# Performance work log

Measured on AMD Instinct MI355X. Metric: run time of the kernel, lower is better.

Reference implementation:

```python
import jax, jax.numpy as jnp
import numpy as np

DIM = 192; HEADS = 6; WS = 7; RES = 56; SHIFT = 3
HEAD_DIM = DIM // HEADS
SCALE = HEAD_DIM ** -0.5
N = WS * WS
EPS = 1e-5

def _rel_pos_index():
    coords = np.stack(np.meshgrid(np.arange(WS), np.arange(WS), indexing='ij')).reshape(2, -1)
    rel = coords[:, :, None] - coords[:, None, :]  # [2,N,N]
    rel = rel.transpose(1, 2, 0)
    rel[:, :, 0] += WS - 1
    rel[:, :, 1] += WS - 1
    rel[:, :, 0] *= 2 * WS - 1
    return rel.sum(-1)  # [N,N]

def _attn_mask():
    img = np.zeros((RES, RES), dtype=np.float32)
    slices = (slice(0, -WS), slice(-WS, -SHIFT), slice(-SHIFT, None))
    cnt = 0
    for h in slices:
        for w in slices:
            img[h, w] = cnt; cnt += 1
    mw = img.reshape(RES // WS, WS, RES // WS, WS).transpose(0, 2, 1, 3).reshape(-1, N)  # [nW,N]
    diff = mw[:, None, :] - mw[:, :, None]
    return np.where(diff != 0, -100.0, 0.0).astype(np.float32)  # [nW,N,N]

REL_IDX = jnp.asarray(_rel_pos_index())
ATTN_MASK = jnp.asarray(_attn_mask())

def _ln(x, g, b):
    mu = x.mean(-1, keepdims=True)
    var = ((x - mu) ** 2).mean(-1, keepdims=True)
    return (x - mu) * jax.lax.rsqrt(var + EPS) * g + b

def setup_inputs() -> dict:
    key = jax.random.key(0)
    ks = jax.random.split(key, 8)
    d = {
        'x': jax.random.normal(ks[0], (32, RES * RES, DIM), jnp.float32),
        'norm1_g': jnp.ones((DIM,), jnp.float32), 'norm1_b': jnp.zeros((DIM,), jnp.float32),
        'qkv_w': jax.random.normal(ks[1], (DIM, 3 * DIM), jnp.float32) * 0.02,
        'qkv_b': jnp.zeros((3 * DIM,), jnp.float32),
        'proj_w': jax.random.normal(ks[2], (DIM, DIM), jnp.float32) * 0.02,
        'proj_b': jnp.zeros((DIM,), jnp.float32),
        'bias_table': jax.random.normal(ks[3], ((2 * WS - 1) ** 2, HEADS), jnp.float32) * 0.02,
        'norm2_g': jnp.ones((DIM,), jnp.float32), 'norm2_b': jnp.zeros((DIM,), jnp.float32),
        'fc1_w': jax.random.normal(ks[4], (DIM, 4 * DIM), jnp.float32) * 0.02,
        'fc1_b': jnp.zeros((4 * DIM,), jnp.float32),
        'fc2_w': jax.random.normal(ks[5], (4 * DIM, DIM), jnp.float32) * 0.02,
        'fc2_b': jnp.zeros((DIM,), jnp.float32),
    }
    return d

def reference(x, norm1_g, norm1_b, qkv_w, qkv_b, proj_w, proj_b, bias_table,
              norm2_g, norm2_b, fc1_w, fc1_b, fc2_w, fc2_b):
    B, L, C = x.shape
    H = W = RES
    shortcut = x
    h = _ln(x, norm1_g, norm1_b).reshape(B, H, W, C)
    # cyclic shift
    h = jnp.roll(h, (-SHIFT, -SHIFT), axis=(1, 2))
    # window partition -> [B*nW, N, C]
    nH = H // WS
    h = h.reshape(B, nH, WS, nH, WS, C).transpose(0, 1, 3, 2, 4, 5).reshape(-1, N, C)
    BW = h.shape[0]
    # windowed MHSA
    qkv = (h @ qkv_w + qkv_b).reshape(BW, N, 3, HEADS, HEAD_DIM)
    q, k, v = qkv[:, :, 0], qkv[:, :, 1], qkv[:, :, 2]  # [BW,N,h,hd]
    attn = jnp.einsum('bnhd,bmhd->bhnm', q, k) * SCALE  # [BW,h,N,N]
    bias = bias_table[REL_IDX.reshape(-1)].reshape(N, N, HEADS).transpose(2, 0, 1)
    attn = attn + bias[None]
    nW = ATTN_MASK.shape[0]
    attn = attn.reshape(BW // nW, nW, HEADS, N, N) + ATTN_MASK[None, :, None]
    attn = jax.nn.softmax(attn.reshape(BW, HEADS, N, N), axis=-1)
    h = jnp.einsum('bhnm,bmhd->bnhd', attn, v).reshape(BW, N, C)
    h = h @ proj_w + proj_b
    # window reverse
    h = h.reshape(B, nH, nH, WS, WS, C).transpose(0, 1, 3, 2, 4, 5).reshape(B, H, W, C)
    h = jnp.roll(h, (SHIFT, SHIFT), axis=(1, 2)).reshape(B, L, C)
    x = shortcut + h
    # MLP
    m = _ln(x, norm2_g, norm2_b)
    m = jax.nn.gelu(m @ fc1_w + fc1_b, approximate=False) @ fc2_w + fc2_b
    return x + m
```

## Files before the change

### kernel.cpp

```cpp
#include <hip/hip_runtime.h>
#include <hip/hip_bf16.h>
#include <math.h>

typedef __attribute__((ext_vector_type(8))) short bh8;
typedef __attribute__((ext_vector_type(4))) float fx4;

__device__ __forceinline__ fx4 mfma_bf16(bh8 a, bh8 b, fx4 c) {
    return __builtin_amdgcn_mfma_f32_16x16x32_bf16(a, b, c, 0, 0, 0);
}

__device__ __forceinline__ void gload16(const __hip_bfloat16* g, __hip_bfloat16* l) {
    __builtin_amdgcn_global_load_lds(
        (const __attribute__((address_space(1))) void*)g,
        (__attribute__((address_space(3))) void*)l,
        16, 0, 0);
}

__device__ __forceinline__ float fast_erf(float u) {
    float au = fabsf(u);
    float t  = __builtin_amdgcn_rcpf(1.0f + 0.3275911f * au);
    float p  = ((((1.061405429f * t - 1.453152027f) * t + 1.421413741f) * t
                 - 0.284496736f) * t + 0.254829592f) * t;
    float e  = __expf(-u * u);
    return copysignf(1.0f - p * e, u);
}

#define WAITV8 do { asm volatile("s_waitcnt vmcnt(8)" ::: "memory"); \
                    __builtin_amdgcn_sched_barrier(0); } while (0)
#define WAITV0 do { asm volatile("s_waitcnt vmcnt(0)" ::: "memory"); \
                    __builtin_amdgcn_sched_barrier(0); } while (0)
#define LGKM0  do { asm volatile("s_waitcnt lgkmcnt(0)" ::: "memory"); \
                    __builtin_amdgcn_sched_barrier(0); } while (0)
#define BARR   do { __builtin_amdgcn_s_barrier(); \
                    __builtin_amdgcn_sched_barrier(0); } while (0)

__global__ __launch_bounds__(256)
void convw_k(const float* __restrict__ W, __hip_bfloat16* __restrict__ Wt, int K, int Nn)
{
    int idx = blockIdx.x * 256 + threadIdx.x;
    if (idx < K * Nn) {
        int k = idx / Nn, n = idx - k * Nn;
        Wt[(size_t)n * K + k] = __float2bfloat16(W[idx]);
    }
}

__global__ __launch_bounds__(256)
void ln1_gather_k(const float* __restrict__ x, const float* __restrict__ g,
                  const float* __restrict__ bia, __hip_bfloat16* __restrict__ xw)
{
    const int wave = threadIdx.x >> 6, lane = threadIdx.x & 63;
    const int t = blockIdx.x * 4 + wave;
    const int w = t / 49, n = t - w * 49;
    const int b = w >> 6, wrem = w & 63, wi = wrem >> 3, wj = wrem & 7;
    const int i = n / 7, j = n - i * 7;
    int sr = wi * 7 + i + 3; if (sr >= 56) sr -= 56;
    int sc = wj * 7 + j + 3; if (sc >= 56) sc -= 56;
    const float* xp = x + ((size_t)b * 3136 + sr * 56 + sc) * 192;
    float v0 = xp[lane], v1 = xp[lane + 64], v2 = xp[lane + 128];
    float s = v0 + v1 + v2;
    float q = v0 * v0 + v1 * v1 + v2 * v2;
    for (int off = 32; off > 0; off >>= 1) {
        s += __shfl_down(s, off, 64);
        q += __shfl_down(q, off, 64);
    }
    s = __shfl(s, 0, 64); q = __shfl(q, 0, 64);
    float mean = s * (1.0f / 192.0f);
    float var  = q * (1.0f / 192.0f) - mean * mean;
    float rstd = rsqrtf(var + 1e-5f);
    __hip_bfloat16* op = xw + (size_t)t * 192;
    op[lane]       = __float2bfloat16((v0 - mean) * rstd * g[lane]       + bia[lane]);
    op[lane + 64]  = __float2bfloat16((v1 - mean) * rstd * g[lane + 64]  + bia[lane + 64]);
    op[lane + 128] = __float2bfloat16((v2 - mean) * rstd * g[lane + 128] + bia[lane + 128]);
}

template<int MODE, int K, int NOUT>
__global__ __launch_bounds__(256)
void gemm2_k(const __hip_bfloat16* __restrict__ A,
             const __hip_bfloat16* __restrict__ Bt,
             const float* __restrict__ bias,
             const float* __restrict__ resid,
             void* __restrict__ outv)
{
    __shared__ __align__(16) __hip_bfloat16 As[128 * 32];
    __shared__ __align__(16) __hip_bfloat16 Bs[64 * 32];
    const int tid  = threadIdx.x;
    const int lane = tid & 63, wave = tid >> 6;
    const int quad = lane >> 4, l15 = lane & 15;
    const int m0 = blockIdx.x * 128, n0 = blockIdx.y * 64;

    const int arow = lane >> 2, acol = (lane & 3) * 8;
    const __hip_bfloat16* Ag0 = A  + (size_t)(m0 + wave * 32 + arow)      * K + acol;
    const __hip_bfloat16* Ag1 = A  + (size_t)(m0 + wave * 32 + 16 + arow) * K + acol;
    const __hip_bfloat16* Bg  = Bt + (size_t)(n0 + wave * 16 + arow)      * K + acol;
    __hip_bfloat16* Al0 = &As[(wave * 32)      * 32];
    __hip_bfloat16* Al1 = &As[(wave * 32 + 16) * 32];
    __hip_bfloat16* Bl  = &Bs[(wave * 16)      * 32];

    fx4 acc[2][4];
#pragma unroll
    for (int mi = 0; mi < 2; mi++)
#pragma unroll
        for (int ni = 0; ni < 4; ni++) acc[mi][ni] = {0.f, 0.f, 0.f, 0.f};

    for (int k0 = 0; k0 < K; k0 += 32) {
        gload16(Ag0 + k0, Al0);
        gload16(Ag1 + k0, Al1);
        gload16(Bg  + k0, Bl);
        __syncthreads();
        bh8 a0 = *(const bh8*)&As[(wave * 32 + l15)      * 32 + quad * 8];
        bh8 a1 = *(const bh8*)&As[(wave * 32 + 16 + l15) * 32 + quad * 8];
        bh8 b0 = *(const bh8*)&Bs[(0 * 16 + l15) * 32 + quad * 8];
        bh8 b1 = *(const bh8*)&Bs[(1 * 16 + l15) * 32 + quad * 8];
        bh8 b2 = *(const bh8*)&Bs[(2 * 16 + l15) * 32 + quad * 8];
        bh8 b3 = *(const bh8*)&Bs[(3 * 16 + l15) * 32 + quad * 8];
        acc[0][0] = mfma_bf16(a0, b0, acc[0][0]);
        acc[0][1] = mfma_bf16(a0, b1, acc[0][1]);
        acc[0][2] = mfma_bf16(a0, b2, acc[0][2]);
        acc[0][3] = mfma_bf16(a0, b3, acc[0][3]);
        acc[1][0] = mfma_bf16(a1, b0, acc[1][0]);
        acc[1][1] = mfma_bf16(a1, b1, acc[1][1]);
        acc[1][2] = mfma_bf16(a1, b2, acc[1][2]);
        acc[1][3] = mfma_bf16(a1, b3, acc[1][3]);
        __syncthreads();
    }

#pragma unroll
    for (int mi = 0; mi < 2; mi++)
#pragma unroll
    for (int ni = 0; ni < 4; ni++) {
        const int n = n0 + ni * 16 + l15;
        const float bn = bias[n];
#pragma unroll
        for (int r = 0; r < 4; r++) {
            const int m = m0 + wave * 32 + mi * 16 + quad * 4 + r;
            float v = acc[mi][ni][r] + bn;
            if (MODE == 0) {
                if (n < 192) v *= 0.17677669529663687f;
                ((__hip_bfloat16*)outv)[(size_t)m * NOUT + n] = __float2bfloat16(v);
            } else if (MODE == 2) {
                v = 0.5f * v * (1.0f + erff(v * 0.70710678118654752f));
                ((__hip_bfloat16*)outv)[(size_t)m * NOUT + n] = __float2bfloat16(v);
            } else {
                ((float*)outv)[(size_t)m * NOUT + n] = v + resid[(size_t)m * NOUT + n];
            }
        }
    }
}

__global__ __launch_bounds__(256)
void mlp_k(const __hip_bfloat16* __restrict__ A,
           const __hip_bfloat16* __restrict__ W1t,
           const __hip_bfloat16* __restrict__ W2t,
           const float* __restrict__ b1,
           const float* __restrict__ b2,
           float* __restrict__ out)
{
    __shared__ __align__(16) __hip_bfloat16 W1s[2][6][32][32];
    __shared__ __align__(16) __hip_bfloat16 W2s[2][192][32];
    __shared__ __align__(16) __hip_bfloat16 Hs[64][40];

    const int tid  = threadIdx.x;
    const int lane = tid & 63, wave = tid >> 6;
    const int quad = lane >> 4, l15 = lane & 15;
    const int m0 = blockIdx.x * 64;
    const int arow = lane >> 2, acol = (lane & 3) * 8;

    bh8 xr[6];
    const __hip_bfloat16* xg = A + (size_t)(m0 + wave * 16 + l15) * 192 + quad * 8;
#pragma unroll
    for (int kc = 0; kc < 6; kc++) xr[kc] = *(const bh8*)(xg + kc * 32);

    auto stage = [&](int bf, int c) {
#pragma unroll
        for (int i = 0; i < 3; i++) {
            const int g = wave * 3 + i;
            const int kc = g >> 1, half = g & 1;
            gload16(W1t + (size_t)(c * 32 + half * 16 + arow) * 192 + kc * 32 + acol,
                    &W1s[bf][kc][half * 16][0]);
            gload16(W2t + (size_t)(g * 16 + arow) * 768 + c * 32 + acol,
                    &W2s[bf][g * 16][0]);
        }
    };

    fx4 acc2[12];
#pragma unroll
    for (int nt = 0; nt < 12; nt++) acc2[nt] = {0.f, 0.f, 0.f, 0.f};

    stage(0, 0);
    float b1a0 = b1[l15],      b1a1 = b1[16 + l15];
    stage(1, 1);
    float b1b0 = b1[32 + l15], b1b1 = b1[48 + l15];
    float b1c0 = 0.f, b1c1 = 0.f;

    int cur = 0;
    for (int c = 0; c < 23; ++c) {
        WAITV8;
        BARR;

        fx4 acc1[2];
        acc1[0] = {0.f, 0.f, 0.f, 0.f};
        acc1[1] = {0.f, 0.f, 0.f, 0.f};
        __builtin_amdgcn_s_setprio(1);
#pragma unroll
        for (int kc = 0; kc < 6; kc++) {
#pragma unroll
            for (int ni = 0; ni < 2; ni++) {
                bh8 b = *(const bh8*)&W1s[cur][kc][ni * 16 + l15][quad * 8];
                acc1[ni] = mfma_bf16(xr[kc], b, acc1[ni]);
            }
        }
        __builtin_amdgcn_s_setprio(0);

#pragma unroll
        for (int ni = 0; ni < 2; ni++) {
            const float bb = ni ? b1a1 : b1a0;
#pragma unroll
            for (int r = 0; r < 4; r++) {
                float v = acc1[ni][r] + bb;
                float h = 0.5f * v * (1.0f + fast_erf(v * 0.70710678118654752f));
                Hs[wave * 16 + quad * 4 + r][ni * 16 + l15] = __float2bfloat16(h);
            }
        }
        LGKM0;

        bh8 ap = *(const bh8*)&Hs[wave * 16 + l15][quad * 8];
        __builtin_amdgcn_s_setprio(1);
#pragma unroll
        for (int nt = 0; nt < 12; nt++) {
            bh8 b = *(const bh8*)&W2s[cur][nt * 16 + l15][quad * 8];
            acc2[nt] = mfma_bf16(ap, b, acc2[nt]);
        }
        __builtin_amdgcn_s_setprio(0);

        BARR;
        if (c < 22) {
            stage(cur, c + 2);
            b1c0 = b1[(c + 2) * 32 + l15];
            b1c1 = b1[(c + 2) * 32 + 16 + l15];
        }
        b1a0 = b1b0; b1a1 = b1b1;
        b1b0 = b1c0; b1b1 = b1c1;
        cur ^= 1;
    }

    {
        WAITV0;
        BARR;
        fx4 acc1[2];
        acc1[0] = {0.f, 0.f, 0.f, 0.f};
        acc1[1] = {0.f, 0.f, 0.f, 0.f};
#pragma unroll
        for (int kc = 0; kc < 6; kc++) {
#pragma unroll
            for (int ni = 0; ni < 2; ni++) {
                bh8 b = *(const bh8*)&W1s[cur][kc][ni * 16 + l15][quad * 8];
                acc1[ni] = mfma_bf16(xr[kc], b, acc1[ni]);
            }
        }
#pragma unroll
        for (int ni = 0; ni < 2; ni++) {
            const float bb = ni ? b1a1 : b1a0;
#pragma unroll
            for (int r = 0; r < 4; r++) {
                float v = acc1[ni][r] + bb;
                float h = 0.5f * v * (1.0f + fast_erf(v * 0.70710678118654752f));
                Hs[wave * 16 + quad * 4 + r][ni * 16 + l15] = __float2bfloat16(h);
            }
        }
        LGKM0;
        bh8 ap = *(const bh8*)&Hs[wave * 16 + l15][quad * 8];
#pragma unroll
        for (int nt = 0; nt < 12; nt++) {
            bh8 b = *(const bh8*)&W2s[cur][nt * 16 + l15][quad * 8];
            acc2[nt] = mfma_bf16(ap, b, acc2[nt]);
        }
    }

#pragma unroll
    for (int nt = 0; nt < 12; nt++) {
        const int n = nt * 16 + l15;
        const float bn = b2[n];
#pragma unroll
        for (int r = 0; r < 4; r++) {
            const int m = m0 + wave * 16 + quad * 4 + r;
            out[(size_t)m * 192 + n] += acc2[nt][r] + bn;
        }
    }
}

__global__ __launch_bounds__(256)
void projln_k(const __hip_bfloat16* __restrict__ A,
              const __hip_bfloat16* __restrict__ Bt,
              const float* __restrict__ pb,
              const float* __restrict__ xresid,
              const float* __restrict__ g2,
              const float* __restrict__ b2,
              float* __restrict__ x1out,
              __hip_bfloat16* __restrict__ y2out)
{
    __shared__ __align__(16) __hip_bfloat16 As[64 * 32];
    __shared__ __align__(16) __hip_bfloat16 Bs[192 * 32];
    const int tid  = threadIdx.x;
    const int lane = tid & 63, wave = tid >> 6;
    const int quad = lane >> 4, l15 = lane & 15;
    const int m0 = blockIdx.x * 64;

    const int arow = lane >> 2, acol = (lane & 3) * 8;
    const __hip_bfloat16* Ag = A + (size_t)(m0 + wave * 16 + arow) * 192 + acol;
    __hip_bfloat16* Al = &As[(wave * 16) * 32];
    const __hip_bfloat16* Bg0 = Bt + (size_t)((wave + 0) * 16 + arow) * 192 + acol;
    const __hip_bfloat16* Bg1 = Bt + (size_t)((wave + 4) * 16 + arow) * 192 + acol;
    const __hip_bfloat16* Bg2 = Bt + (size_t)((wave + 8) * 16 + arow) * 192 + acol;
    __hip_bfloat16* Bl0 = &Bs[((wave + 0) * 16) * 32];
    __hip_bfloat16* Bl1 = &Bs[((wave + 4) * 16) * 32];
    __hip_bfloat16* Bl2 = &Bs[((wave + 8) * 16) * 32];

    fx4 acc[12];
#pragma unroll
    for (int ct = 0; ct < 12; ct++) acc[ct] = {0.f, 0.f, 0.f, 0.f};

    for (int k0 = 0; k0 < 192; k0 += 32) {
        gload16(Ag  + k0, Al);
        gload16(Bg0 + k0, Bl0);
        gload16(Bg1 + k0, Bl1);
        gload16(Bg2 + k0, Bl2);
        __syncthreads();
        bh8 a = *(const bh8*)&As[(wave * 16 + l15) * 32 + quad * 8];
#pragma unroll
        for (int ct = 0; ct < 12; ct++) {
            bh8 b = *(const bh8*)&Bs[(ct * 16 + l15) * 32 + quad * 8];
            acc[ct] = mfma_bf16(a, b, acc[ct]);
        }
        __syncthreads();
    }

#pragma unroll
    for (int r = 0; r < 4; r++) {
        const int row = m0 + wave * 16 + quad * 4 + r;
        float vv[12];
        float s = 0.f, q = 0.f;
#pragma unroll
        for (int ct = 0; ct < 12; ct++) {
            const int col = ct * 16 + l15;
            float v = acc[ct][r] + pb[col] + xresid[(size_t)row * 192 + col];
            vv[ct] = v;
            x1out[(size_t)row * 192 + col] = v;
            s += v;
            q += v * v;
        }
        s += __shfl_xor(s, 1, 64);  q += __shfl_xor(q, 1, 64);
        s += __shfl_xor(s, 2, 64);  q += __shfl_xor(q, 2, 64);
        s += __shfl_xor(s, 4, 64);  q += __shfl_xor(q, 4, 64);
        s += __shfl_xor(s, 8, 64);  q += __shfl_xor(q, 8, 64);
        float mean = s * (1.0f / 192.0f);
        float var  = q * (1.0f / 192.0f) - mean * mean;
        float rstd = rsqrtf(var + 1e-5f);
#pragma unroll
        for (int ct = 0; ct < 12; ct++) {
            const int col = ct * 16 + l15;
            float y = (vv[ct] - mean) * rstd * g2[col] + b2[col];
            y2out[(size_t)row * 192 + col] = __float2bfloat16(y);
        }
    }
}

__global__ __launch_bounds__(256)
void attn_k(const __hip_bfloat16* __restrict__ qkv,
            const float* __restrict__ bias_table,
            __hip_bfloat16* __restrict__ aout)
{
    __shared__ __align__(16) __hip_bfloat16 Qb[64 * 32];
    __shared__ __align__(16) __hip_bfloat16 Kb[64 * 32];
    __shared__ __align__(16) __hip_bfloat16 Vt[32 * 64];
    __shared__ __align__(16) __hip_bfloat16 Ps[64 * 72];
    __shared__ float bias_h[169];

    const int tid  = threadIdx.x;
    const int lane = tid & 63, wave = tid >> 6;
    const int quad = lane >> 4, l15 = lane & 15;
    const int w = blockIdx.x / 6, hd = blockIdx.x % 6;
    const int b = w >> 6, wrem = w & 63, wi = wrem >> 3, wj = wrem & 7;
    const size_t base = (size_t)w * 49 * 576 + hd * 32;

    if (tid < 169) bias_h[tid] = bias_table[tid * 6 + hd];

    bh8 z = {0, 0, 0, 0, 0, 0, 0, 0};
    {
        int row = tid >> 2, ch = (tid & 3) * 8;
        if (row < 49) {
            *(bh8*)&Qb[row * 32 + ch] = *(const bh8*)(qkv + base + (size_t)row * 576 + ch);
            *(bh8*)&Kb[row * 32 + ch] = *(const bh8*)(qkv + base + (size_t)row * 576 + 192 + ch);
        } else {
            *(bh8*)&Qb[row * 32 + ch] = z;
            *(bh8*)&Kb[row * 32 + ch] = z;
        }
        *(bh8*)&Vt[tid * 8] = z;
    }
    __syncthreads();
    for (int idx = tid; idx < 49 * 32; idx += 256) {
        int n = idx >> 5, d = idx & 31;
        Vt[d * 64 + n] = qkv[base + (size_t)n * 576 + 384 + d];
    }
    __syncthreads();

    fx4 zf = {0.f, 0.f, 0.f, 0.f};
    bh8 aq = *(const bh8*)&Qb[(wave * 16 + l15) * 32 + quad * 8];
    fx4 sarr[4];
#pragma unroll
    for (int ni = 0; ni < 4; ni++) {
        bh8 bk = *(const bh8*)&Kb[(ni * 16 + l15) * 32 + quad * 8];
        sarr[ni] = mfma_bf16(aq, bk, zf);
    }

    int iarr[4], ria[4], cia[4], mbi[4];
#pragma unroll
    for (int r = 0; r < 4; r++) {
        int i = wave * 16 + quad * 4 + r;
        int ri = i / 7, ci = i - ri * 7;
        iarr[r] = i; ria[r] = ri; cia[r] = ci;
        int ar = wi * 7 + ri, ac = wj * 7 + ci;
        int br = (ar < 49) ? 0 : ((ar < 53) ? 1 : 2);
        int bc = (ac < 49) ? 0 : ((ac < 53) ? 1 : 2);
        mbi[r] = br * 3 + bc;
    }
    float vals[4][4];
#pragma unroll
    for (int ni = 0; ni < 4; ni++) {
        int jcol = ni * 16 + l15;
        int rj = jcol / 7, cj = jcol - rj * 7;
        int ar = wi * 7 + rj, ac = wj * 7 + cj;
        int br = (ar < 49) ? 0 : ((ar < 53) ? 1 : 2);
        int bc = (ac < 49) ? 0 : ((ac < 53) ? 1 : 2);
        int mbj = br * 3 + bc;
#pragma unroll
        for (int r = 0; r < 4; r++) {
            float v;
            if (jcol >= 49)            v = -1e30f;
            else if (iarr[r] >= 49)    v = 0.0f;
            else {
                int bidx = (ria[r] - rj + 6) * 13 + (cia[r] - cj + 6);
                v = sarr[ni][r] + bias_h[bidx] + ((mbi[r] != mbj) ? -100.0f : 0.0f);
            }
            vals[ni][r] = v;
        }
    }
#pragma unroll
    for (int r = 0; r < 4; r++) {
        float mx = fmaxf(fmaxf(vals[0][r], vals[1][r]), fmaxf(vals[2][r], vals[3][r]));
        mx = fmaxf(mx, __shfl_xor(mx, 1, 64));
        mx = fmaxf(mx, __shfl_xor(mx, 2, 64));
        mx = fmaxf(mx, __shfl_xor(mx, 4, 64));
        mx = fmaxf(mx, __shfl_xor(mx, 8, 64));
        float e0 = __expf(vals[0][r] - mx);
        float e1 = __expf(vals[1][r] - mx);
        float e2 = __expf(vals[2][r] - mx);
        float e3 = __expf(vals[3][r] - mx);
        float sm = e0 + e1 + e2 + e3;
        sm += __shfl_xor(sm, 1, 64);
        sm += __shfl_xor(sm, 2, 64);
        sm += __shfl_xor(sm, 4, 64);
        sm += __shfl_xor(sm, 8, 64);
        float inv = 1.0f / sm;
        int prow = (wave * 16 + quad * 4 + r) * 72;
        Ps[prow + 0 * 16 + l15] = __float2bfloat16(e0 * inv);
        Ps[prow + 1 * 16 + l15] = __float2bfloat16(e1 * inv);
        Ps[prow + 2 * 16 + l15] = __float2bfloat16(e2 * inv);
        Ps[prow + 3 * 16 + l15] = __float2bfloat16(e3 * inv);
    }
    __syncthreads();

    fx4 o0 = zf, o1 = zf;
#pragma unroll
    for (int k0 = 0; k0 < 64; k0 += 32) {
        bh8 ap  = *(const bh8*)&Ps[(wave * 16 + l15) * 72 + k0 + quad * 8];
        bh8 bv0 = *(const bh8*)&Vt[(l15)      * 64 + k0 + quad * 8];
        bh8 bv1 = *(const bh8*)&Vt[(16 + l15) * 64 + k0 + quad * 8];
        o0 = mfma_bf16(ap, bv0, o0);
        o1 = mfma_bf16(ap, bv1, o1);
    }

#pragma unroll
    for (int r = 0; r < 4; r++) {
        int m = wave * 16 + quad * 4 + r;
        if (m < 49) {
            int i = m / 7, j2 = m - i * 7;
            int orow = wi * 7 + i + 3;  if (orow >= 56) orow -= 56;
            int ocol = wj * 7 + j2 + 3; if (ocol >= 56) ocol -= 56;
            size_t t = (size_t)b * 3136 + orow * 56 + ocol;
            aout[t * 192 + hd * 32 + l15]      = __float2bfloat16(o0[r]);
            aout[t * 192 + hd * 32 + 16 + l15] = __float2bfloat16(o1[r]);
        }
    }
}

extern "C" void kernel_launch(void* const* d_in, const int* in_sizes, int n_in,
                              void* d_out, int out_size, void* d_ws, size_t ws_size,
                              hipStream_t stream)
{
    const float* x      = (const float*)d_in[0];
    const float* n1g    = (const float*)d_in[1];
    const float* n1b    = (const float*)d_in[2];
    const float* qkv_w  = (const float*)d_in[3];
    const float* qkv_b  = (const float*)d_in[4];
    const float* proj_w = (const float*)d_in[5];
    const float* proj_b = (const float*)d_in[6];
    const float* btab   = (const float*)d_in[7];
    const float* n2g    = (const float*)d_in[8];
    const float* n2b    = (const float*)d_in[9];
    const float* fc1_w  = (const float*)d_in[10];
    const float* fc1_b  = (const float*)d_in[11];
    const float* fc2_w  = (const float*)d_in[12];
    const float* fc2_b  = (const float*)d_in[13];

    char* ws = (char*)d_ws;
    __hip_bfloat16* buf1    = (__hip_bfloat16*)(ws + 0);
    __hip_bfloat16* buf2    = (__hip_bfloat16*)(ws + 38535168);
    __hip_bfloat16* wt_qkv  = (__hip_bfloat16*)(ws + 192675840);
    __hip_bfloat16* wt_proj = (__hip_bfloat16*)(ws + 192897024);
    __hip_bfloat16* wt_fc1  = (__hip_bfloat16*)(ws + 192970752);
    __hip_bfloat16* wt_fc2  = (__hip_bfloat16*)(ws + 193265664);
    float*          x1      = (float*)d_out;

    convw_k<<<dim3(432), 256, 0, stream>>>(qkv_w, wt_qkv, 192, 576);
    convw_k<<<dim3(144), 256, 0, stream>>>(proj_w, wt_proj, 192, 192);
    convw_k<<<dim3(576), 256, 0, stream>>>(fc1_w, wt_fc1, 192, 768);
    convw_k<<<dim3(576), 256, 0, stream>>>(fc2_w, wt_fc2, 768, 192);

    ln1_gather_k<<<dim3(25088), 256, 0, stream>>>(x, n1g, n1b, buf1);

    gemm2_k<0, 192, 576><<<dim3(784, 9), 256, 0, stream>>>(buf1, wt_qkv, qkv_b, nullptr, buf2);

    attn_k<<<dim3(12288), 256, 0, stream>>>(buf2, btab, buf1);

    projln_k<<<dim3(1568), 256, 0, stream>>>(buf1, wt_proj, proj_b, x, n2g, n2b, x1, buf1);

    mlp_k<<<dim3(1568), 256, 0, stream>>>(buf1, wt_fc1, wt_fc2, fc1_b, fc2_b, x1);
}
```

Measured before the change: 536.0 us.

## Double MLP block rows to 128 so each staged weight tile feeds twice the work

The fused MLP kernel now handles 128 rows per block, with each wave owning two 16-row tiles. Each weight fragment read from LDS therefore feeds two MFMAs, and the fc1/fc2 weight streaming per output row is halved, with half as many blocks launched. The fc1 bias is preloaded into shared memory instead of being fetched every chunk, and the GELU output is written to LDS as packed 4-element stores by swapping the MFMA operand order so the transposed layout fits. Register pressure roughly doubles for the accumulators, and a launch bound of 2 blocks per SIMD group is requested, which risks spills and lower occupancy.

Result: faster. 482.7 us (-9.9%).

```diff
diff --git a/kernel.cpp b/kernel.cpp
--- a/kernel.cpp
+++ b/kernel.cpp
@@ -3,6 +3,7 @@
 #include <math.h>
 
 typedef __attribute__((ext_vector_type(8))) short bh8;
+typedef __attribute__((ext_vector_type(4))) short sh4;
 typedef __attribute__((ext_vector_type(4))) float fx4;
 
 __device__ __forceinline__ fx4 mfma_bf16(bh8 a, bh8 b, fx4 c) {
@@ -25,7 +26,7 @@
     return copysignf(1.0f - p * e, u);
 }
 
-#define WAITV8 do { asm volatile("s_waitcnt vmcnt(8)" ::: "memory"); \
+#define WAITV6 do { asm volatile("s_waitcnt vmcnt(6)" ::: "memory"); \
                     __builtin_amdgcn_sched_barrier(0); } while (0)
 #define WAITV0 do { asm volatile("s_waitcnt vmcnt(0)" ::: "memory"); \
                     __builtin_amdgcn_sched_barrier(0); } while (0)
@@ -147,7 +148,7 @@
     }
 }
 
-__global__ __launch_bounds__(256)
+__global__ __launch_bounds__(256, 2)
 void mlp_k(const __hip_bfloat16* __restrict__ A,
            const __hip_bfloat16* __restrict__ W1t,
            const __hip_bfloat16* __restrict__ W2t,
@@ -157,18 +158,25 @@
 {
     __shared__ __align__(16) __hip_bfloat16 W1s[2][6][32][32];
     __shared__ __align__(16) __hip_bfloat16 W2s[2][192][32];
-    __shared__ __align__(16) __hip_bfloat16 Hs[64][40];
+    __shared__ __align__(16) __hip_bfloat16 Hs[128][40];
+    __shared__ __align__(16) float b1s[768];
 
     const int tid  = threadIdx.x;
     const int lane = tid & 63, wave = tid >> 6;
     const int quad = lane >> 4, l15 = lane & 15;
-    const int m0 = blockIdx.x * 64;
+    const int m0 = blockIdx.x * 128;
     const int arow = lane >> 2, acol = (lane & 3) * 8;
 
-    bh8 xr[6];
-    const __hip_bfloat16* xg = A + (size_t)(m0 + wave * 16 + l15) * 192 + quad * 8;
-#pragma unroll
-    for (int kc = 0; kc < 6; kc++) xr[kc] = *(const bh8*)(xg + kc * 32);
+    if (tid < 192) ((fx4*)b1s)[tid] = ((const fx4*)b1)[tid];
+    LGKM0;
+
+    bh8 xr[2][6];
+    const __hip_bfloat16* xg = A + (size_t)(m0 + wave * 32 + l15) * 192 + quad * 8;
+#pragma unroll
+    for (int rt = 0; rt < 2; rt++)
+#pragma unroll
+        for (int kc = 0; kc < 6; kc++)
+            xr[rt][kc] = *(const bh8*)(xg + rt * 16 * 192 + kc * 32);
 
     auto stage = [&](int bf, int c) {
 #pragma unroll
@@ -182,108 +190,128 @@
         }
     };
 
-    fx4 acc2[12];
-#pragma unroll
-    for (int nt = 0; nt < 12; nt++) acc2[nt] = {0.f, 0.f, 0.f, 0.f};
+    fx4 acc2[2][12];
+#pragma unroll
+    for (int rt = 0; rt < 2; rt++)
+#pragma unroll
+        for (int nt = 0; nt < 12; nt++) acc2[rt][nt] = {0.f, 0.f, 0.f, 0.f};
 
     stage(0, 0);
-    float b1a0 = b1[l15],      b1a1 = b1[16 + l15];
     stage(1, 1);
-    float b1b0 = b1[32 + l15], b1b1 = b1[48 + l15];
-    float b1c0 = 0.f, b1c1 = 0.f;
 
     int cur = 0;
     for (int c = 0; c < 23; ++c) {
-        WAITV8;
+        WAITV6;
         BARR;
 
-        fx4 acc1[2];
-        acc1[0] = {0.f, 0.f, 0.f, 0.f};
-        acc1[1] = {0.f, 0.f, 0.f, 0.f};
+        fx4 bv0 = *(const fx4*)&b1s[c * 32 + 0 * 16 + quad * 4];
+        fx4 bv1 = *(const fx4*)&b1s[c * 32 + 1 * 16 + quad * 4];
+
+        fx4 acc1[2][2];
+        acc1[0][0] = {0.f, 0.f, 0.f, 0.f}; acc1[0][1] = {0.f, 0.f, 0.f, 0.f};
+        acc1[1][0] = {0.f, 0.f, 0.f, 0.f}; acc1[1][1] = {0.f, 0.f, 0.f, 0.f};
         __builtin_amdgcn_s_setprio(1);
 #pragma unroll
         for (int kc = 0; kc < 6; kc++) {
 #pragma unroll
             for (int ni = 0; ni < 2; ni++) {
-                bh8 b = *(const bh8*)&W1s[cur][kc][ni * 16 + l15][quad * 8];
-                acc1[ni] = mfma_bf16(xr[kc], b, acc1[ni]);
+                bh8 w = *(const bh8*)&W1s[cur][kc][ni * 16 + l15][quad * 8];
+                acc1[0][ni] = mfma_bf16(w, xr[0][kc], acc1[0][ni]);
+                acc1[1][ni] = mfma_bf16(w, xr[1][kc], acc1[1][ni]);
             }
         }
         __builtin_amdgcn_s_setprio(0);
 
 #pragma unroll
-        for (int ni = 0; ni < 2; ni++) {
-            const float bb = ni ? b1a1 : b1a0;
-#pragma unroll
-            for (int r = 0; r < 4; r++) {
-                float v = acc1[ni][r] + bb;
-                float h = 0.5f * v * (1.0f + fast_erf(v * 0.70710678118654752f));
-                Hs[wave * 16 + quad * 4 + r][ni * 16 + l15] = __float2bfloat16(h);
+        for (int rt = 0; rt < 2; rt++) {
+#pragma unroll
+            for (int ni = 0; ni < 2; ni++) {
+                const fx4 bv = ni ? bv1 : bv0;
+                sh4 pk;
+#pragma unroll
+                for (int r = 0; r < 4; r++) {
+                    float v = acc1[rt][ni][r] + bv[r];
+                    float h = 0.5f * v * (1.0f + fast_erf(v * 0.70710678118654752f));
+                    union { __hip_bfloat16 hb; short s; } u;
+                    u.hb = __float2bfloat16(h);
+                    pk[r] = u.s;
+                }
+                *(sh4*)&Hs[wave * 32 + rt * 16 + l15][ni * 16 + quad * 4] = pk;
             }
         }
         LGKM0;
 
-        bh8 ap = *(const bh8*)&Hs[wave * 16 + l15][quad * 8];
+        bh8 ha0 = *(const bh8*)&Hs[wave * 32 + l15][quad * 8];
+        bh8 ha1 = *(const bh8*)&Hs[wave * 32 + 16 + l15][quad * 8];
         __builtin_amdgcn_s_setprio(1);
 #pragma unroll
         for (int nt = 0; nt < 12; nt++) {
-            bh8 b = *(const bh8*)&W2s[cur][nt * 16 + l15][quad * 8];
-            acc2[nt] = mfma_bf16(ap, b, acc2[nt]);
+            bh8 w2 = *(const bh8*)&W2s[cur][nt * 16 + l15][quad * 8];
+            acc2[0][nt] = mfma_bf16(ha0, w2, acc2[0][nt]);
+            acc2[1][nt] = mfma_bf16(ha1, w2, acc2[1][nt]);
         }
         __builtin_amdgcn_s_setprio(0);
 
         BARR;
-        if (c < 22) {
-            stage(cur, c + 2);
-            b1c0 = b1[(c + 2) * 32 + l15];
-            b1c1 = b1[(c + 2) * 32 + 16 + l15];
-        }
-        b1a0 = b1b0; b1a1 = b1b1;
-        b1b0 = b1c0; b1b1 = b1c1;
+        if (c < 22) stage(cur, c + 2);
         cur ^= 1;
     }
 
     {
         WAITV0;
         BARR;
-        fx4 acc1[2];
-        acc1[0] = {0.f, 0.f, 0.f, 0.f};
-        acc1[1] = {0.f, 0.f, 0.f, 0.f};
+        fx4 bv0 = *(const fx4*)&b1s[23 * 32 + 0 * 16 + quad * 4];
+        fx4 bv1 = *(const fx4*)&b1s[23 * 32 + 1 * 16 + quad * 4];
+        fx4 acc1[2][2];
+        acc1[0][0] = {0.f, 0.f, 0.f, 0.f}; acc1[0][1] = {0.f, 0.f, 0.f, 0.f};
+        acc1[1][0] = {0.f, 0.f, 0.f, 0.f}; acc1[1][1] = {0.f, 0.f, 0.f, 0.f};
 #pragma unroll
         for (int kc = 0; kc < 6; kc++) {
 #pragma unroll
             for (int ni = 0; ni < 2; ni++) {
-                bh8 b = *(const bh8*)&W1s[cur][kc][ni * 16 + l15][quad * 8];
-                acc1[ni] = mfma_bf16(xr[kc], b, acc1[ni]);
+                bh8 w = *(const bh8*)&W1s[cur][kc][ni * 16 + l15][quad * 8];
+                acc1[0][ni] = mfma_bf16(w, xr[0][kc], acc1[0][ni]);
+                acc1[1][ni] = mfma_bf16(w, xr[1][kc], acc1[1][ni]);
             }
         }
 #pragma unroll
-        for (int ni = 0; ni < 2; ni++) {
-            const float bb = ni ? b1a1 : b1a0;
-#pragma unroll
-            for (int r = 0; r < 4; r++) {
-                float v = acc1[ni][r] + bb;
-                float h = 0.5f * v * (1.0f + fast_erf(v * 0.70710678118654752f));
-                Hs[wave * 16 + quad * 4 + r][ni * 16 + l15] = __float2bfloat16(h);
+        for (int rt = 0; rt < 2; rt++) {
+#pragma unroll
+            for (int ni = 0; ni < 2; ni++) {
+                const fx4 bv = ni ? bv1 : bv0;
+                sh4 pk;
+#pragma unroll
+                for (int r = 0; r < 4; r++) {
+                    float v = acc1[rt][ni][r] + bv[r];
+                    float h = 0.5f * v * (1.0f + fast_erf(v * 0.70710678118654752f));
+                    union { __hip_bfloat16 hb; short s; } u;
+                    u.hb = __float2bfloat16(h);
+                    pk[r] = u.s;
+                }
+                *(sh4*)&Hs[wave * 32 + rt * 16 + l15][ni * 16 + quad * 4] = pk;
             }
         }
         LGKM0;
-        bh8 ap = *(const bh8*)&Hs[wave * 16 + l15][quad * 8];
+        bh8 ha0 = *(const bh8*)&Hs[wave * 32 + l15][quad * 8];
+        bh8 ha1 = *(const bh8*)&Hs[wave * 32 + 16 + l15][quad * 8];
 #pragma unroll
         for (int nt = 0; nt < 12; nt++) {
-            bh8 b = *(const bh8*)&W2s[cur][nt * 16 + l15][quad * 8];
-            acc2[nt] = mfma_bf16(ap, b, acc2[nt]);
-        }
-    }
-
+            bh8 w2 = *(const bh8*)&W2s[cur][nt * 16 + l15][quad * 8];
+            acc2[0][nt] = mfma_bf16(ha0, w2, acc2[0][nt]);
+            acc2[1][nt] = mfma_bf16(ha1, w2, acc2[1][nt]);
+        }
+    }
+
+#pragma unroll
+    for (int rt = 0; rt < 2; rt++)
 #pragma unroll
     for (int nt = 0; nt < 12; nt++) {
         const int n = nt * 16 + l15;
         const float bn = b2[n];
 #pragma unroll
         for (int r = 0; r < 4; r++) {
-            const int m = m0 + wave * 16 + quad * 4 + r;
-            out[(size_t)m * 192 + n] += acc2[nt][r] + bn;
+            const int m = m0 + wave * 32 + rt * 16 + quad * 4 + r;
+            out[(size_t)m * 192 + n] += acc2[rt][nt][r] + bn;
         }
     }
 }
@@ -534,5 +562,5 @@
 
     projln_k<<<dim3(1568), 256, 0, stream>>>(buf1, wt_proj, proj_b, x, n2g, n2b, x1, buf1);
 
-    mlp_k<<<dim3(1568), 256, 0, stream>>>(buf1, wt_fc1, wt_fc2, fc1_b, fc2_b, x1);
-}
+    mlp_k<<<dim3(784), 256, 0, stream>>>(buf1, wt_fc1, wt_fc2, fc1_b, fc2_b, x1);
+}
```
